# Optimization experiments

Measured on AMD Instinct MI355X. Metric: run time of the kernel, lower is better.

## Reference

```python
import jax, jax.numpy as jnp
import numpy as np

NUM_HEADS = 8

def setup_inputs() -> dict:
    key = jax.random.key(0)
    ks = jax.random.split(key, 6)
    B, S, D, K = 2, 2048, 512, 64
    x = jax.random.normal(ks[0], (B, S, D), dtype=jnp.float32)
    routes = jax.random.randint(ks[1], (S, K), 0, S, dtype=jnp.int32)
    distances = jax.random.uniform(ks[2], (S, S), dtype=jnp.float32)
    W_in = jax.random.normal(ks[3], (D, D), dtype=jnp.float32) * (1.0 / np.sqrt(D))
    W_out = jax.random.normal(ks[4], (D, D), dtype=jnp.float32) * (1.0 / np.sqrt(D))
    b_out = jnp.zeros((D,), dtype=jnp.float32)
    return {"x": x, "routes": routes, "distances": distances,
            "W_in": W_in, "W_out": W_out, "b_out": b_out}

def reference(x, routes, distances, W_in, W_out, b_out):
    # x: [B,S,D]; routes: [S,K] int gather table; distances: [S,S]
    B, S, D = x.shape
    H = NUM_HEADS
    hd = D // H
    K = routes.shape[1]
    # in_proj (torch Linear, no bias): y = x @ W^T
    h = jnp.einsum('bsd,ed->bse', x, W_in).reshape(B, S, H, hd)
    # gather fusion windows via precomputed routes: [B,S,K,H,hd]
    gathered = h[:, routes]
    # weighted fusion: weights from precomputed Cantor distance matrix
    d = jnp.take_along_axis(distances, routes.astype(jnp.int32), axis=1)  # [S,K]
    w = jax.nn.softmax(-d, axis=-1)  # normalized fusion weights
    fused = jnp.einsum('sk,bskhd->bshd', w, gathered)  # [B,S,H,hd]
    fused = fused.reshape(B, S, D)
    # out_proj + residual (dropout is identity in eval)
    out = jnp.einsum('bsd,ed->bse', fused, W_out) + b_out
    return out + x
```

## Files before the change

### kernel.cpp

```cpp
#include <hip/hip_runtime.h>
#include <hip/hip_bf16.h>

#define S_DIM 2048
#define D_DIM 512
#define B_DIM 2
#define K_RT  64
#define M_DIM 4096

typedef __attribute__((ext_vector_type(8))) short short8;
typedef __attribute__((ext_vector_type(4))) float f32x4;
typedef unsigned int u32;
#define AS1 __attribute__((address_space(1)))
#define AS3 __attribute__((address_space(3)))

static __device__ __forceinline__ float bf16lo_to_f(unsigned u) {
    union { unsigned u; float f; } c; c.u = u << 16; return c.f;
}
static __device__ __forceinline__ float bf16hi_to_f(unsigned u) {
    union { unsigned u; float f; } c; c.u = u & 0xffff0000u; return c.f;
}
static __device__ __forceinline__ unsigned short f_to_bf16(float f) {
    union { float f; unsigned u; } c; c.f = f;
    unsigned u = c.u;
    u += 0x7fffu + ((u >> 16) & 1u);
    return (unsigned short)(u >> 16);
}
static __device__ __forceinline__ unsigned pk2(float a, float b) {
    return (unsigned)f_to_bf16(a) | ((unsigned)f_to_bf16(b) << 16);
}

__global__ __launch_bounds__(256) void prep(
    const float* __restrict__ x, const int* __restrict__ routes,
    const float* __restrict__ distances,
    const float* __restrict__ Wi, const float* __restrict__ Wo,
    unsigned short* __restrict__ xb, unsigned short* __restrict__ wib,
    unsigned short* __restrict__ wob, float* __restrict__ w)
{
    const int blk = blockIdx.x;
    if (blk < 512) {
        const int lane = threadIdx.x & 63;
        const int wv   = threadIdx.x >> 6;
        const int s    = blk * 4 + wv;
        const int rt   = routes[s * K_RT + lane];
        const float v  = -distances[(size_t)s * S_DIM + rt];
        float mx = v;
        #pragma unroll
        for (int off = 32; off >= 1; off >>= 1) mx = fmaxf(mx, __shfl_xor(mx, off, 64));
        const float e = __expf(v - mx);
        float sum = e;
        #pragma unroll
        for (int off = 32; off >= 1; off >>= 1) sum += __shfl_xor(sum, off, 64);
        w[s * K_RT + lane] = e / sum;
    } else {
        const int g = (blk - 512) * 256 + threadIdx.x;
        const int NX = M_DIM * D_DIM / 4;
        const int NW = D_DIM * D_DIM / 4;
        const float* src; unsigned short* dst; int off;
        if (g < NX)           { src = x;  dst = xb;  off = g; }
        else if (g < NX + NW) { src = Wi; dst = wib; off = g - NX; }
        else                  { src = Wo; dst = wob; off = g - NX - NW; }
        const float4 v = ((const float4*)src)[off];
        ushort4 o;
        o.x = f_to_bf16(v.x); o.y = f_to_bf16(v.y);
        o.z = f_to_bf16(v.z); o.w = f_to_bf16(v.w);
        ((ushort4*)dst)[off] = o;
    }
}

#define GBM 64
#define GBN 64
#define GBK 32

template<bool OUTF32>
__global__ __launch_bounds__(256) void gemm_bt(
    const unsigned short* __restrict__ A,
    const unsigned short* __restrict__ B,
    void* __restrict__ Cv,
    const float* __restrict__ bias, const float* __restrict__ residual,
    int M, int N, int K)
{
    __shared__ unsigned short As[GBM * GBK];
    __shared__ unsigned short Bs[GBN * GBK];

    const int tid  = threadIdx.x;
    const int lane = tid & 63;
    const int wv   = tid >> 6;
    const int wm   = (wv & 1) * 32;
    const int wn   = (wv >> 1) * 32;
    const int m0   = blockIdx.y * GBM;
    const int n0   = blockIdx.x * GBN;

    const int srow  = wv * 16 + (lane >> 2);
    const int skoff = (lane & 3) * 8;

    const int mi = lane & 15;
    const int kg = lane >> 4;

    f32x4 acc[2][2] = {};

    for (int k0 = 0; k0 < K; k0 += GBK) {
        __builtin_amdgcn_global_load_lds(
            (const AS1 u32*)(A + (size_t)(m0 + srow) * K + k0 + skoff),
            (AS3 u32*)(As + wv * 16 * GBK), 16, 0, 0);
        __builtin_amdgcn_global_load_lds(
            (const AS1 u32*)(B + (size_t)(n0 + srow) * K + k0 + skoff),
            (AS3 u32*)(Bs + wv * 16 * GBK), 16, 0, 0);
        __syncthreads();

        short8 af0 = *(const short8*)(As + (wm +      mi) * GBK + kg * 8);
        short8 af1 = *(const short8*)(As + (wm + 16 + mi) * GBK + kg * 8);
        short8 bf0 = *(const short8*)(Bs + (wn +      mi) * GBK + kg * 8);
        short8 bf1 = *(const short8*)(Bs + (wn + 16 + mi) * GBK + kg * 8);

        acc[0][0] = __builtin_amdgcn_mfma_f32_16x16x32_bf16(af0, bf0, acc[0][0], 0, 0, 0);
        acc[0][1] = __builtin_amdgcn_mfma_f32_16x16x32_bf16(af0, bf1, acc[0][1], 0, 0, 0);
        acc[1][0] = __builtin_amdgcn_mfma_f32_16x16x32_bf16(af1, bf0, acc[1][0], 0, 0, 0);
        acc[1][1] = __builtin_amdgcn_mfma_f32_16x16x32_bf16(af1, bf1, acc[1][1], 0, 0, 0);
        __syncthreads();
    }

    const int rb  = (lane >> 4) * 4;
    const int col = lane & 15;
    #pragma unroll
    for (int i = 0; i < 2; ++i) {
        #pragma unroll
        for (int j = 0; j < 2; ++j) {
            #pragma unroll
            for (int r = 0; r < 4; ++r) {
                const int m = m0 + wm + i * 16 + rb + r;
                const int n = n0 + wn + j * 16 + col;
                const float v = acc[i][j][r];
                if (OUTF32) {
                    ((float*)Cv)[(size_t)m * N + n] = v + bias[n] + residual[(size_t)m * N + n];
                } else {
                    ((unsigned short*)Cv)[(size_t)m * N + n] = f_to_bf16(v);
                }
            }
        }
    }
}

__global__ __launch_bounds__(256) void fuse_gather(
    const unsigned short* __restrict__ h, const int* __restrict__ routes,
    const float* __restrict__ w, unsigned short* __restrict__ fused)
{
    const int tid  = threadIdx.x;
    const int lane = tid & 63;
    const int wv   = tid >> 6;
    const int bx   = blockIdx.x;
    const int b    = bx & 1;
    const int s    = (bx >> 1) * 4 + wv;

    const int   rt = routes[s * K_RT + lane];
    const float wl = w[s * K_RT + lane];

    const unsigned short* hb = h + (size_t)b * S_DIM * D_DIM;
    float acc[8] = {};
    #pragma unroll
    for (int k = 0; k < 64; ++k) {
        const int   rk = __builtin_amdgcn_readlane(rt, k);
        const float wk = __int_as_float(__builtin_amdgcn_readlane(__float_as_int(wl), k));
        const uint4 p = *(const uint4*)(hb + (size_t)rk * D_DIM + lane * 8);
        acc[0] = fmaf(wk, bf16lo_to_f(p.x), acc[0]);
        acc[1] = fmaf(wk, bf16hi_to_f(p.x), acc[1]);
        acc[2] = fmaf(wk, bf16lo_to_f(p.y), acc[2]);
        acc[3] = fmaf(wk, bf16hi_to_f(p.y), acc[3]);
        acc[4] = fmaf(wk, bf16lo_to_f(p.z), acc[4]);
        acc[5] = fmaf(wk, bf16hi_to_f(p.z), acc[5]);
        acc[6] = fmaf(wk, bf16lo_to_f(p.w), acc[6]);
        acc[7] = fmaf(wk, bf16hi_to_f(p.w), acc[7]);
    }
    uint4 o;
    o.x = pk2(acc[0], acc[1]);
    o.y = pk2(acc[2], acc[3]);
    o.z = pk2(acc[4], acc[5]);
    o.w = pk2(acc[6], acc[7]);
    *(uint4*)(fused + ((size_t)b * S_DIM + s) * D_DIM + lane * 8) = o;
}

extern "C" void kernel_launch(void* const* d_in, const int* in_sizes, int n_in,
                              void* d_out, int out_size, void* d_ws, size_t ws_size,
                              hipStream_t stream) {
    const float* x         = (const float*)d_in[0];
    const int*   routes    = (const int*)  d_in[1];
    const float* distances = (const float*)d_in[2];
    const float* W_in      = (const float*)d_in[3];
    const float* W_out     = (const float*)d_in[4];
    const float* b_out     = (const float*)d_in[5];
    float* out = (float*)d_out;

    unsigned short* xb  = (unsigned short*)d_ws;
    unsigned short* wib = xb  + (size_t)M_DIM * D_DIM;
    unsigned short* wob = wib + (size_t)D_DIM * D_DIM;
    unsigned short* hb  = wob + (size_t)D_DIM * D_DIM;
    unsigned short* fb  = hb  + (size_t)M_DIM * D_DIM;
    float*          w   = (float*)(fb + (size_t)M_DIM * D_DIM);

    const dim3 ggrid(D_DIM / GBN, M_DIM / GBM);

    prep<<<3072, 256, 0, stream>>>(x, routes, distances, W_in, W_out, xb, wib, wob, w);
    gemm_bt<false><<<ggrid, 256, 0, stream>>>(xb, wib, hb, nullptr, nullptr, M_DIM, D_DIM, D_DIM);
    fuse_gather<<<dim3(1024), 256, 0, stream>>>(hb, routes, w, fb);
    gemm_bt<true><<<ggrid, 256, 0, stream>>>(fb, wob, out, b_out, x, M_DIM, D_DIM, D_DIM);
}
```

Measured before the change: 111.9 us.

## Fuse softmax weights into gather kernel and double GEMM K-tile per barrier

Softmax weight computation moves out of the prep kernel into fuse_gather, so the intermediate weight buffer is no longer written and re-read, and prep shrinks to a pure cast kernel. Each batch recomputes the softmax, so the distance gather and reductions run twice. The GEMM now loads two 32-wide K slices per iteration into separate LDS buffers, which halves the number of barrier pairs and loop iterations. The cost is more LDS per block.

```diff
diff --git a/kernel.cpp b/kernel.cpp
--- a/kernel.cpp
+++ b/kernel.cpp
@@ -29,47 +29,28 @@
     return (unsigned)f_to_bf16(a) | ((unsigned)f_to_bf16(b) << 16);
 }
 
-__global__ __launch_bounds__(256) void prep(
-    const float* __restrict__ x, const int* __restrict__ routes,
-    const float* __restrict__ distances,
-    const float* __restrict__ Wi, const float* __restrict__ Wo,
+__global__ __launch_bounds__(256) void prep_cast(
+    const float* __restrict__ x, const float* __restrict__ Wi, const float* __restrict__ Wo,
     unsigned short* __restrict__ xb, unsigned short* __restrict__ wib,
-    unsigned short* __restrict__ wob, float* __restrict__ w)
+    unsigned short* __restrict__ wob)
 {
-    const int blk = blockIdx.x;
-    if (blk < 512) {
-        const int lane = threadIdx.x & 63;
-        const int wv   = threadIdx.x >> 6;
-        const int s    = blk * 4 + wv;
-        const int rt   = routes[s * K_RT + lane];
-        const float v  = -distances[(size_t)s * S_DIM + rt];
-        float mx = v;
-        #pragma unroll
-        for (int off = 32; off >= 1; off >>= 1) mx = fmaxf(mx, __shfl_xor(mx, off, 64));
-        const float e = __expf(v - mx);
-        float sum = e;
-        #pragma unroll
-        for (int off = 32; off >= 1; off >>= 1) sum += __shfl_xor(sum, off, 64);
-        w[s * K_RT + lane] = e / sum;
-    } else {
-        const int g = (blk - 512) * 256 + threadIdx.x;
-        const int NX = M_DIM * D_DIM / 4;
-        const int NW = D_DIM * D_DIM / 4;
-        const float* src; unsigned short* dst; int off;
-        if (g < NX)           { src = x;  dst = xb;  off = g; }
-        else if (g < NX + NW) { src = Wi; dst = wib; off = g - NX; }
-        else                  { src = Wo; dst = wob; off = g - NX - NW; }
-        const float4 v = ((const float4*)src)[off];
-        ushort4 o;
-        o.x = f_to_bf16(v.x); o.y = f_to_bf16(v.y);
-        o.z = f_to_bf16(v.z); o.w = f_to_bf16(v.w);
-        ((ushort4*)dst)[off] = o;
-    }
+    const int g = blockIdx.x * 256 + threadIdx.x;
+    const int NX = M_DIM * D_DIM / 4;
+    const int NW = D_DIM * D_DIM / 4;
+    const float* src; unsigned short* dst; int off;
+    if (g < NX)           { src = x;  dst = xb;  off = g; }
+    else if (g < NX + NW) { src = Wi; dst = wib; off = g - NX; }
+    else                  { src = Wo; dst = wob; off = g - NX - NW; }
+    const float4 v = ((const float4*)src)[off];
+    ushort4 o;
+    o.x = f_to_bf16(v.x); o.y = f_to_bf16(v.y);
+    o.z = f_to_bf16(v.z); o.w = f_to_bf16(v.w);
+    ((ushort4*)dst)[off] = o;
 }
 
 #define GBM 64
 #define GBN 64
-#define GBK 32
+#define GBK 64
 
 template<bool OUTF32>
 __global__ __launch_bounds__(256) void gemm_bt(
@@ -79,8 +60,8 @@
     const float* __restrict__ bias, const float* __restrict__ residual,
     int M, int N, int K)
 {
-    __shared__ unsigned short As[GBM * GBK];
-    __shared__ unsigned short Bs[GBN * GBK];
+    __shared__ unsigned short As[2][GBM * 32];
+    __shared__ unsigned short Bs[2][GBN * 32];
 
     const int tid  = threadIdx.x;
     const int lane = tid & 63;
@@ -99,23 +80,30 @@
     f32x4 acc[2][2] = {};
 
     for (int k0 = 0; k0 < K; k0 += GBK) {
-        __builtin_amdgcn_global_load_lds(
-            (const AS1 u32*)(A + (size_t)(m0 + srow) * K + k0 + skoff),
-            (AS3 u32*)(As + wv * 16 * GBK), 16, 0, 0);
-        __builtin_amdgcn_global_load_lds(
-            (const AS1 u32*)(B + (size_t)(n0 + srow) * K + k0 + skoff),
-            (AS3 u32*)(Bs + wv * 16 * GBK), 16, 0, 0);
+        const size_t arow = (size_t)(m0 + srow) * K + k0 + skoff;
+        const size_t brow = (size_t)(n0 + srow) * K + k0 + skoff;
+        __builtin_amdgcn_global_load_lds((const AS1 u32*)(A + arow),
+                                         (AS3 u32*)(As[0] + wv * 512), 16, 0, 0);
+        __builtin_amdgcn_global_load_lds((const AS1 u32*)(A + arow + 32),
+                                         (AS3 u32*)(As[1] + wv * 512), 16, 0, 0);
+        __builtin_amdgcn_global_load_lds((const AS1 u32*)(B + brow),
+                                         (AS3 u32*)(Bs[0] + wv * 512), 16, 0, 0);
+        __builtin_amdgcn_global_load_lds((const AS1 u32*)(B + brow + 32),
+                                         (AS3 u32*)(Bs[1] + wv * 512), 16, 0, 0);
         __syncthreads();
 
-        short8 af0 = *(const short8*)(As + (wm +      mi) * GBK + kg * 8);
-        short8 af1 = *(const short8*)(As + (wm + 16 + mi) * GBK + kg * 8);
-        short8 bf0 = *(const short8*)(Bs + (wn +      mi) * GBK + kg * 8);
-        short8 bf1 = *(const short8*)(Bs + (wn + 16 + mi) * GBK + kg * 8);
-
-        acc[0][0] = __builtin_amdgcn_mfma_f32_16x16x32_bf16(af0, bf0, acc[0][0], 0, 0, 0);
-        acc[0][1] = __builtin_amdgcn_mfma_f32_16x16x32_bf16(af0, bf1, acc[0][1], 0, 0, 0);
-        acc[1][0] = __builtin_amdgcn_mfma_f32_16x16x32_bf16(af1, bf0, acc[1][0], 0, 0, 0);
-        acc[1][1] = __builtin_amdgcn_mfma_f32_16x16x32_bf16(af1, bf1, acc[1][1], 0, 0, 0);
+        #pragma unroll
+        for (int kh = 0; kh < 2; ++kh) {
+            short8 af0 = *(const short8*)(As[kh] + (wm +      mi) * 32 + kg * 8);
+            short8 af1 = *(const short8*)(As[kh] + (wm + 16 + mi) * 32 + kg * 8);
+            short8 bf0 = *(const short8*)(Bs[kh] + (wn +      mi) * 32 + kg * 8);
+            short8 bf1 = *(const short8*)(Bs[kh] + (wn + 16 + mi) * 32 + kg * 8);
+
+            acc[0][0] = __builtin_amdgcn_mfma_f32_16x16x32_bf16(af0, bf0, acc[0][0], 0, 0, 0);
+            acc[0][1] = __builtin_amdgcn_mfma_f32_16x16x32_bf16(af0, bf1, acc[0][1], 0, 0, 0);
+            acc[1][0] = __builtin_amdgcn_mfma_f32_16x16x32_bf16(af1, bf0, acc[1][0], 0, 0, 0);
+            acc[1][1] = __builtin_amdgcn_mfma_f32_16x16x32_bf16(af1, bf1, acc[1][1], 0, 0, 0);
+        }
         __syncthreads();
     }
 
@@ -142,7 +130,7 @@
 
 __global__ __launch_bounds__(256) void fuse_gather(
     const unsigned short* __restrict__ h, const int* __restrict__ routes,
-    const float* __restrict__ w, unsigned short* __restrict__ fused)
+    const float* __restrict__ distances, unsigned short* __restrict__ fused)
 {
     const int tid  = threadIdx.x;
     const int lane = tid & 63;
@@ -151,8 +139,16 @@
     const int b    = bx & 1;
     const int s    = (bx >> 1) * 4 + wv;
 
-    const int   rt = routes[s * K_RT + lane];
-    const float wl = w[s * K_RT + lane];
+    const int rt = routes[s * K_RT + lane];
+    const float v = -distances[(size_t)s * S_DIM + rt];
+    float mx = v;
+    #pragma unroll
+    for (int off = 32; off >= 1; off >>= 1) mx = fmaxf(mx, __shfl_xor(mx, off, 64));
+    const float e = __expf(v - mx);
+    float sum = e;
+    #pragma unroll
+    for (int off = 32; off >= 1; off >>= 1) sum += __shfl_xor(sum, off, 64);
+    const float wl = e / sum;
 
     const unsigned short* hb = h + (size_t)b * S_DIM * D_DIM;
     float acc[8] = {};
@@ -194,12 +190,11 @@
     unsigned short* wob = wib + (size_t)D_DIM * D_DIM;
     unsigned short* hb  = wob + (size_t)D_DIM * D_DIM;
     unsigned short* fb  = hb  + (size_t)M_DIM * D_DIM;
-    float*          w   = (float*)(fb + (size_t)M_DIM * D_DIM);
 
     const dim3 ggrid(D_DIM / GBN, M_DIM / GBM);
 
-    prep<<<3072, 256, 0, stream>>>(x, routes, distances, W_in, W_out, xb, wib, wob, w);
+    prep_cast<<<2560, 256, 0, stream>>>(x, W_in, W_out, xb, wib, wob);
     gemm_bt<false><<<ggrid, 256, 0, stream>>>(xb, wib, hb, nullptr, nullptr, M_DIM, D_DIM, D_DIM);
-    fuse_gather<<<dim3(1024), 256, 0, stream>>>(hb, routes, w, fb);
+    fuse_gather<<<dim3(1024), 256, 0, stream>>>(hb, routes, distances, fb);
     gemm_bt<true><<<ggrid, 256, 0, stream>>>(fb, wob, out, b_out, x, M_DIM, D_DIM, D_DIM);
 }
```

After: 111.6 us. No clear change (-0.3%).
